# Performance work log

Hardware: AMD Instinct MI355X
Metric: run time of the kernel (lower is better)

The kernel has to match this reference:

```python
import jax, jax.numpy as jnp
import numpy as np

C = 64

def conv1x1(x, w, b):
    # x: [..., C, H, W], w: [C_out, C_in], b: [C_out]  (1x1 conv == channel mix)
    return jnp.einsum('oi,...ihw->...ohw', w, x) + b[:, None, None]

def setup_inputs() -> dict:
    key = jax.random.key(0)
    ks = jax.random.split(key, 8)
    B, N, H, W = 4, 4, 256, 256
    s = 1.0 / np.sqrt(C)
    return {
        'main_input': jax.random.normal(ks[0], (B, C, H, W), jnp.float32),
        'assist_inputs': jax.random.normal(ks[1], (N, B, C, H, W), jnp.float32),
        'wq': jax.random.normal(ks[2], (C, C), jnp.float32) * s,
        'bq': jax.random.normal(ks[3], (C,), jnp.float32) * 0.01,
        'wk': jax.random.normal(ks[4], (C, C), jnp.float32) * s,
        'bk': jax.random.normal(ks[5], (C,), jnp.float32) * 0.01,
        'wv': jax.random.normal(ks[6], (C, C), jnp.float32) * s,
        'bv': jax.random.normal(ks[7], (C,), jnp.float32) * 0.01,
    }

def reference(main_input, assist_inputs, wq, bq, wk, bk, wv, bv):
    H, W = main_input.shape[-2], main_input.shape[-1]
    q = conv1x1(main_input, wq, bq)          # [B,C,H,W]
    v = conv1x1(main_input, wv, bv)          # [B,C,H,W] (same every loop iter)
    k = conv1x1(assist_inputs, wk, bk)       # [N,B,C,H,W]
    # time-axis attention: q @ k^T over W -> [N,B,C,H,H]
    attn_t = jax.nn.softmax(jnp.einsum('bchw,nbcgw->nbchg', q, k) / jnp.sqrt(jnp.float32(H)), axis=-1)
    time_ctx = jnp.einsum('nbchg,bcgw->nbchw', attn_t, v)
    # channel(space)-axis attention: q^T @ k over H -> [N,B,C,W,W]
    attn_s = jax.nn.softmax(jnp.einsum('bchw,nbchv->nbcwv', q, k) / jnp.sqrt(jnp.float32(W)), axis=-1)
    sc_ctx = jnp.einsum('bchw,nbcwv->nbchv', v, attn_s)
    return main_input + jnp.sum(time_ctx + sc_ctx, axis=0)
```

## Files before the change

kernel.cpp:

```cpp
#include <hip/hip_runtime.h>

#define HW 65536
#define CDIM 64

typedef __attribute__((ext_vector_type(8))) short bf16x8;
typedef __attribute__((ext_vector_type(4))) float f32x4;
typedef __attribute__((ext_vector_type(4))) unsigned short u16x4;

__device__ __forceinline__ unsigned short f2bf(float x) {
    union { float f; unsigned u; } v; v.f = x;
    unsigned r = v.u + 0x7fffu + ((v.u >> 16) & 1u);
    return (unsigned short)(r >> 16);
}


__global__ __launch_bounds__(256, 2)
void proj_qv_kernel(const float* __restrict__ x,
                    const float* __restrict__ wq, const float* __restrict__ bq,
                    const float* __restrict__ wv, const float* __restrict__ bv,
                    unsigned short* __restrict__ qo, unsigned short* __restrict__ vo) {
    const int t = threadIdx.x;
    const int b = blockIdx.y;
    const int pix = blockIdx.x * 256 + t;
    const float* xp = x + (size_t)b * CDIM * HW + pix;

    float aq[CDIM], av[CDIM];
#pragma unroll
    for (int c = 0; c < CDIM; ++c) { aq[c] = bq[c]; av[c] = bv[c]; }

    for (int i = 0; i < CDIM; ++i) {
        float xv = xp[(size_t)i * HW];
#pragma unroll
        for (int c = 0; c < CDIM; ++c) {
            aq[c] = fmaf(wq[c * CDIM + i], xv, aq[c]);
            av[c] = fmaf(wv[c * CDIM + i], xv, av[c]);
        }
    }
    size_t ob = (size_t)b * CDIM * HW + pix;
#pragma unroll
    for (int c = 0; c < CDIM; ++c) {
        qo[ob + (size_t)c * HW] = f2bf(aq[c]);
        vo[ob + (size_t)c * HW] = f2bf(av[c]);
    }
}

__global__ __launch_bounds__(256, 2)
void proj_k_kernel(const float* __restrict__ x,
                   const float* __restrict__ wk, const float* __restrict__ bk,
                   unsigned short* __restrict__ ko) {
    const int t = threadIdx.x;
    const int nb = blockIdx.y;
    const int pix = blockIdx.x * 256 + t;
    const float* xp = x + (size_t)nb * CDIM * HW + pix;

    float ak[CDIM];
#pragma unroll
    for (int c = 0; c < CDIM; ++c) ak[c] = bk[c];

    for (int i = 0; i < CDIM; ++i) {
        float xv = xp[(size_t)i * HW];
#pragma unroll
        for (int c = 0; c < CDIM; ++c) ak[c] = fmaf(wk[c * CDIM + i], xv, ak[c]);
    }
    size_t ob = (size_t)nb * CDIM * HW + pix;
#pragma unroll
    for (int c = 0; c < CDIM; ++c) ko[ob + (size_t)c * HW] = f2bf(ak[c]);
}


__global__ __launch_bounds__(256)
void transpose_kernel(const unsigned short* __restrict__ src, unsigned short* __restrict__ dst) {
    __shared__ unsigned short T[64 * 72];
    const int t = threadIdx.x;
    const int sl = blockIdx.y;
    const int th = blockIdx.x >> 2, tw = blockIdx.x & 3;

    const unsigned short* s = src + (size_t)sl * HW + th * 64 * 256 + tw * 64;
#pragma unroll
    for (int it = 0; it < 2; ++it) {
        int cc = t + it * 256;
        int r = cc >> 3, j = cc & 7;
        *(bf16x8*)&T[r * 72 + j * 8] = *(const bf16x8*)&s[r * 256 + j * 8];
    }
    __syncthreads();
    unsigned short* d = dst + (size_t)sl * HW + tw * 64 * 256 + th * 64;
#pragma unroll
    for (int it = 0; it < 2; ++it) {
        int cc = t + it * 256;
        int w = cc >> 3, j = cc & 7;
        bf16x8 val;
#pragma unroll
        for (int e = 0; e < 8; ++e) val[e] = (short)T[(j * 8 + e) * 72 + w];
        *(bf16x8*)&d[w * 256 + j * 8] = val;
    }
}

#define PSTRIDE 264
#define KBOFF   67584
#define KBSTRIDE 40

__global__ __launch_bounds__(512, 2)
void attn_kernel(const unsigned short* __restrict__ q,  const unsigned short* __restrict__ qT,
                 const unsigned short* __restrict__ v,  const unsigned short* __restrict__ vT,
                 const unsigned short* __restrict__ k,  const unsigned short* __restrict__ kT,
                 const float* __restrict__ mainx, float* __restrict__ out) {
    __shared__ unsigned short lds[77824];

    const int t = threadIdx.x;
    const int wave = t >> 6, lane = t & 63;
    const int quad = lane >> 4, l16 = lane & 15;
    const int bc = blockIdx.x;

    const unsigned short* Q  = q  + (size_t)bc * HW;
    const unsigned short* QT = qT + (size_t)bc * HW;
    const unsigned short* V  = v  + (size_t)bc * HW;
    const unsigned short* VT = vT + (size_t)bc * HW;

    f32x4 oacc[2][16];
#pragma unroll
    for (int rt = 0; rt < 2; ++rt)
#pragma unroll
        for (int ct = 0; ct < 16; ++ct) oacc[rt][ct] = (f32x4){0.f, 0.f, 0.f, 0.f};

    auto stage = [&](const unsigned short* src, int col0) {
#pragma unroll
        for (int it = 0; it < 2; ++it) {
            int cc = t + it * 512;
            int r = cc >> 2, j = cc & 3;
            *(bf16x8*)&lds[KBOFF + r * KBSTRIDE + j * 8] =
                *(const bf16x8*)&src[r * 256 + col0 + j * 8];
        }
    };

    for (int n = 0; n < 4; ++n) {
        const unsigned short* K  = k  + ((size_t)n * 256 + bc) * HW;
        const unsigned short* KT = kT + ((size_t)n * 256 + bc) * HW;

        for (int rt = 0; rt < 2; ++rt) {
            f32x4 s[16];
#pragma unroll
            for (int ct = 0; ct < 16; ++ct) s[ct] = (f32x4){0.f, 0.f, 0.f, 0.f};
            const unsigned short* arow = Q + (wave * 32 + rt * 16 + l16) * 256 + quad * 8;
            for (int ks = 0; ks < 8; ++ks) {
                __syncthreads();
                stage(K, ks * 32);
                __syncthreads();
                bf16x8 a = *(const bf16x8*)&arow[ks * 32];
#pragma unroll
                for (int ct = 0; ct < 16; ++ct) {
                    bf16x8 bb = *(const bf16x8*)&lds[KBOFF + (ct * 16 + l16) * KBSTRIDE + quad * 8];
                    s[ct] = __builtin_amdgcn_mfma_f32_16x16x32_bf16(a, bb, s[ct], 0, 0, 0);
                }
            }
#pragma unroll
            for (int r = 0; r < 4; ++r) {
                float m = s[0][r];
#pragma unroll
                for (int ct = 1; ct < 16; ++ct) m = fmaxf(m, s[ct][r]);
#pragma unroll
                for (int off = 1; off < 16; off <<= 1) m = fmaxf(m, __shfl_xor(m, off, 64));
                float sum = 0.f;
#pragma unroll
                for (int ct = 0; ct < 16; ++ct) {
                    float e = __expf((s[ct][r] - m) * 0.0625f);
                    s[ct][r] = e; sum += e;
                }
#pragma unroll
                for (int off = 1; off < 16; off <<= 1) sum += __shfl_xor(sum, off, 64);
                float inv = 1.f / sum;
#pragma unroll
                for (int ct = 0; ct < 16; ++ct) s[ct][r] *= inv;
            }
            int hh = wave * 32 + rt * 16 + quad * 4;
#pragma unroll
            for (int ct = 0; ct < 16; ++ct)
#pragma unroll
                for (int r = 0; r < 4; ++r)
                    lds[(hh + r) * PSTRIDE + ct * 16 + l16] = f2bf(s[ct][r]);
        }
        __syncthreads();
        for (int gb = 0; gb < 8; ++gb) {
            __syncthreads();
            stage(VT, gb * 32);
            __syncthreads();
#pragma unroll
            for (int rt = 0; rt < 2; ++rt) {
                bf16x8 a = *(const bf16x8*)&lds[(wave * 32 + rt * 16 + l16) * PSTRIDE + gb * 32 + quad * 8];
#pragma unroll
                for (int ct = 0; ct < 16; ++ct) {
                    bf16x8 bb = *(const bf16x8*)&lds[KBOFF + (ct * 16 + l16) * KBSTRIDE + quad * 8];
                    oacc[rt][ct] = __builtin_amdgcn_mfma_f32_16x16x32_bf16(a, bb, oacc[rt][ct], 0, 0, 0);
                }
            }
        }

        for (int rt = 0; rt < 2; ++rt) {
            f32x4 s[16];
#pragma unroll
            for (int ct = 0; ct < 16; ++ct) s[ct] = (f32x4){0.f, 0.f, 0.f, 0.f};
            const unsigned short* arow = QT + (wave * 32 + rt * 16 + l16) * 256 + quad * 8;
            for (int ks = 0; ks < 8; ++ks) {
                __syncthreads();
                stage(KT, ks * 32);
                __syncthreads();
                bf16x8 a = *(const bf16x8*)&arow[ks * 32];
#pragma unroll
                for (int ct = 0; ct < 16; ++ct) {
                    bf16x8 bb = *(const bf16x8*)&lds[KBOFF + (ct * 16 + l16) * KBSTRIDE + quad * 8];
                    s[ct] = __builtin_amdgcn_mfma_f32_16x16x32_bf16(a, bb, s[ct], 0, 0, 0);
                }
            }
#pragma unroll
            for (int r = 0; r < 4; ++r) {
                float m = s[0][r];
#pragma unroll
                for (int ct = 1; ct < 16; ++ct) m = fmaxf(m, s[ct][r]);
#pragma unroll
                for (int off = 1; off < 16; off <<= 1) m = fmaxf(m, __shfl_xor(m, off, 64));
                float sum = 0.f;
#pragma unroll
                for (int ct = 0; ct < 16; ++ct) {
                    float e = __expf((s[ct][r] - m) * 0.0625f);
                    s[ct][r] = e; sum += e;
                }
#pragma unroll
                for (int off = 1; off < 16; off <<= 1) sum += __shfl_xor(sum, off, 64);
                float inv = 1.f / sum;
#pragma unroll
                for (int ct = 0; ct < 16; ++ct) s[ct][r] *= inv;
            }
            int wbase = wave * 32 + rt * 16 + quad * 4;
#pragma unroll
            for (int ct = 0; ct < 16; ++ct) {
                u16x4 pk;
#pragma unroll
                for (int r = 0; r < 4; ++r) pk[r] = f2bf(s[ct][r]);
                *(u16x4*)&lds[(ct * 16 + l16) * PSTRIDE + wbase] = pk;
            }
        }
        __syncthreads();
        for (int ks = 0; ks < 8; ++ks) {
#pragma unroll
            for (int rt = 0; rt < 2; ++rt) {
                bf16x8 a = *(const bf16x8*)&V[(wave * 32 + rt * 16 + l16) * 256 + ks * 32 + quad * 8];
#pragma unroll
                for (int ct = 0; ct < 16; ++ct) {
                    bf16x8 bb = *(const bf16x8*)&lds[(ct * 16 + l16) * PSTRIDE + ks * 32 + quad * 8];
                    oacc[rt][ct] = __builtin_amdgcn_mfma_f32_16x16x32_bf16(a, bb, oacc[rt][ct], 0, 0, 0);
                }
            }
        }
        __syncthreads();
    }

    const float* mp = mainx + (size_t)bc * HW;
    float* op = out + (size_t)bc * HW;
#pragma unroll
    for (int rt = 0; rt < 2; ++rt)
#pragma unroll
        for (int ct = 0; ct < 16; ++ct)
#pragma unroll
            for (int r = 0; r < 4; ++r) {
                int hh = wave * 32 + rt * 16 + quad * 4 + r;
                int ww = ct * 16 + l16;
                op[hh * 256 + ww] = mp[hh * 256 + ww] + oacc[rt][ct][r];
            }
}


extern "C" void kernel_launch(void* const* d_in, const int* in_sizes, int n_in,
                              void* d_out, int out_size, void* d_ws, size_t ws_size,
                              hipStream_t stream) {
    const float* mainx  = (const float*)d_in[0];
    const float* assist = (const float*)d_in[1];
    const float* wq = (const float*)d_in[2];
    const float* bq = (const float*)d_in[3];
    const float* wk = (const float*)d_in[4];
    const float* bk = (const float*)d_in[5];
    const float* wv = (const float*)d_in[6];
    const float* bv = (const float*)d_in[7];
    float* outp = (float*)d_out;

    unsigned short* ws = (unsigned short*)d_ws;
    const size_t SLICE = (size_t)16777216;
    unsigned short* Qw  = ws;
    unsigned short* QTw = ws + SLICE;
    unsigned short* Vw  = ws + 2 * SLICE;
    unsigned short* VTw = ws + 3 * SLICE;
    unsigned short* Kw  = ws + 4 * SLICE;
    unsigned short* KTw = ws + 8 * SLICE;

    proj_qv_kernel<<<dim3(256, 4), 256, 0, stream>>>(mainx, wq, bq, wv, bv, Qw, Vw);
    proj_k_kernel<<<dim3(256, 16), 256, 0, stream>>>(assist, wk, bk, Kw);

    transpose_kernel<<<dim3(16, 256), 256, 0, stream>>>(Qw, QTw);
    transpose_kernel<<<dim3(16, 256), 256, 0, stream>>>(Vw, VTw);
    transpose_kernel<<<dim3(16, 1024), 256, 0, stream>>>(Kw, KTw);

    attn_kernel<<<dim3(256), 512, 0, stream>>>(Qw, QTw, Vw, VTw, Kw, KTw, mainx, outp);
}
```

Before: 1.143 ms.

## Rewrite projections and attention with register-tiled MFMA and max-free softmax

The projection kernels are replaced by a single register-tiled kernel that keeps transposed weights in LDS and computes an 8x8 channel-by-pixel block per thread with vectorized loads. The attention kernel now splits work across waves in a 2x4 grid with 4x4 MFMA sub-tiles loaded straight from global memory, dropping the per-step LDS staging of K and its double barriers. Softmax no longer subtracts the row max: it exponentiates, accumulates partial sums through LDS, then rescales P in place. This removes barriers and the max reduction, but risks overflow if scores grow large and adds an extra LDS rescale pass.

New measurement: 1.378 ms. +20.5%, slower.

```diff
diff --git a/kernel.cpp b/kernel.cpp
--- a/kernel.cpp
+++ b/kernel.cpp
@@ -2,71 +2,78 @@
 
 #define HW 65536
 #define CDIM 64
+#define PST 264
 
 typedef __attribute__((ext_vector_type(8))) short bf16x8;
 typedef __attribute__((ext_vector_type(4))) float f32x4;
 typedef __attribute__((ext_vector_type(4))) unsigned short u16x4;
+typedef __attribute__((ext_vector_type(8))) unsigned short u16x8;
 
 __device__ __forceinline__ unsigned short f2bf(float x) {
     union { float f; unsigned u; } v; v.f = x;
     unsigned r = v.u + 0x7fffu + ((v.u >> 16) & 1u);
     return (unsigned short)(r >> 16);
 }
-
-
-__global__ __launch_bounds__(256, 2)
-void proj_qv_kernel(const float* __restrict__ x,
-                    const float* __restrict__ wq, const float* __restrict__ bq,
-                    const float* __restrict__ wv, const float* __restrict__ bv,
-                    unsigned short* __restrict__ qo, unsigned short* __restrict__ vo) {
+__device__ __forceinline__ float bf2f(unsigned short u) {
+    union { unsigned u; float f; } v; v.u = ((unsigned)u) << 16; return v.f;
+}
+
+__global__ __launch_bounds__(256, 4)
+void proj_kernel(const float* __restrict__ x, const float* __restrict__ w,
+                 const float* __restrict__ bias, unsigned short* __restrict__ o) {
+    __shared__ float WT[64 * 68];
     const int t = threadIdx.x;
-    const int b = blockIdx.y;
-    const int pix = blockIdx.x * 256 + t;
-    const float* xp = x + (size_t)b * CDIM * HW + pix;
-
-    float aq[CDIM], av[CDIM];
-#pragma unroll
-    for (int c = 0; c < CDIM; ++c) { aq[c] = bq[c]; av[c] = bv[c]; }
-
-    for (int i = 0; i < CDIM; ++i) {
-        float xv = xp[(size_t)i * HW];
-#pragma unroll
-        for (int c = 0; c < CDIM; ++c) {
-            aq[c] = fmaf(wq[c * CDIM + i], xv, aq[c]);
-            av[c] = fmaf(wv[c * CDIM + i], xv, av[c]);
-        }
-    }
-    size_t ob = (size_t)b * CDIM * HW + pix;
-#pragma unroll
-    for (int c = 0; c < CDIM; ++c) {
-        qo[ob + (size_t)c * HW] = f2bf(aq[c]);
-        vo[ob + (size_t)c * HW] = f2bf(av[c]);
-    }
-}
-
-__global__ __launch_bounds__(256, 2)
-void proj_k_kernel(const float* __restrict__ x,
-                   const float* __restrict__ wk, const float* __restrict__ bk,
-                   unsigned short* __restrict__ ko) {
-    const int t = threadIdx.x;
-    const int nb = blockIdx.y;
-    const int pix = blockIdx.x * 256 + t;
-    const float* xp = x + (size_t)nb * CDIM * HW + pix;
-
-    float ak[CDIM];
-#pragma unroll
-    for (int c = 0; c < CDIM; ++c) ak[c] = bk[c];
-
-    for (int i = 0; i < CDIM; ++i) {
-        float xv = xp[(size_t)i * HW];
-#pragma unroll
-        for (int c = 0; c < CDIM; ++c) ak[c] = fmaf(wk[c * CDIM + i], xv, ak[c]);
-    }
-    size_t ob = (size_t)nb * CDIM * HW + pix;
-#pragma unroll
-    for (int c = 0; c < CDIM; ++c) ko[ob + (size_t)c * HW] = f2bf(ak[c]);
-}
-
+    const int slice = blockIdx.y;
+    const int pixbase = blockIdx.x * 256;
+    const int tc = t >> 5, tp = t & 31;
+    const int c0 = tc * 8, p0 = pixbase + tp * 8;
+
+#pragma unroll
+    for (int it = 0; it < 16; ++it) {
+        int idx = it * 256 + t;
+        int c = idx >> 6, i = idx & 63;
+        WT[i * 68 + c] = w[idx];
+    }
+    __syncthreads();
+
+    const float* xb = x + (size_t)slice * CDIM * HW;
+    float acc[8][8];
+#pragma unroll
+    for (int cc = 0; cc < 8; ++cc) {
+        float b = bias[c0 + cc];
+#pragma unroll
+        for (int pp = 0; pp < 8; ++pp) acc[cc][pp] = b;
+    }
+
+#pragma unroll 2
+    for (int i = 0; i < 64; ++i) {
+        f32x4 x0 = *(const f32x4*)&xb[(size_t)i * HW + p0];
+        f32x4 x1 = *(const f32x4*)&xb[(size_t)i * HW + p0 + 4];
+        f32x4 w0 = *(const f32x4*)&WT[i * 68 + c0];
+        f32x4 w1 = *(const f32x4*)&WT[i * 68 + c0 + 4];
+#pragma unroll
+        for (int cc = 0; cc < 4; ++cc) {
+#pragma unroll
+            for (int pp = 0; pp < 4; ++pp) {
+                acc[cc][pp]     = fmaf(w0[cc], x0[pp], acc[cc][pp]);
+                acc[cc][pp + 4] = fmaf(w0[cc], x1[pp], acc[cc][pp + 4]);
+                acc[cc + 4][pp]     = fmaf(w1[cc], x0[pp], acc[cc + 4][pp]);
+                acc[cc + 4][pp + 4] = fmaf(w1[cc], x1[pp], acc[cc + 4][pp + 4]);
+            }
+        }
+    }
+
+    unsigned short* ob = o + (size_t)slice * CDIM * HW;
+#pragma unroll
+    for (int cc = 0; cc < 8; ++cc) {
+        u16x4 lo, hi;
+#pragma unroll
+        for (int e = 0; e < 4; ++e) { lo[e] = f2bf(acc[cc][e]); hi[e] = f2bf(acc[cc][e + 4]); }
+        size_t ob2 = (size_t)(c0 + cc) * HW + p0;
+        *(u16x4*)&ob[ob2] = lo;
+        *(u16x4*)&ob[ob2 + 4] = hi;
+    }
+}
 
 __global__ __launch_bounds__(256)
 void transpose_kernel(const unsigned short* __restrict__ src, unsigned short* __restrict__ dst) {
@@ -95,20 +102,20 @@
     }
 }
 
-#define PSTRIDE 264
-#define KBOFF   67584
-#define KBSTRIDE 40
-
 __global__ __launch_bounds__(512, 2)
 void attn_kernel(const unsigned short* __restrict__ q,  const unsigned short* __restrict__ qT,
                  const unsigned short* __restrict__ v,  const unsigned short* __restrict__ vT,
-                 const unsigned short* __restrict__ k,  const unsigned short* __restrict__ kT,
+                 const unsigned short* __restrict__ kk, const unsigned short* __restrict__ kT,
                  const float* __restrict__ mainx, float* __restrict__ out) {
-    __shared__ unsigned short lds[77824];
+    __shared__ unsigned short P[256 * PST];
+    __shared__ float stats[256 * 4];
+    __shared__ float invbuf[264];
 
     const int t = threadIdx.x;
     const int wave = t >> 6, lane = t & 63;
     const int quad = lane >> 4, l16 = lane & 15;
+    const int wr = wave >> 2, wc = wave & 3;
+    const int h0 = wc * 64;
     const int bc = blockIdx.x;
 
     const unsigned short* Q  = q  + (size_t)bc * HW;
@@ -116,141 +123,203 @@
     const unsigned short* V  = v  + (size_t)bc * HW;
     const unsigned short* VT = vT + (size_t)bc * HW;
 
-    f32x4 oacc[2][16];
+    f32x4 oacc[2][4][4];
 #pragma unroll
     for (int rt = 0; rt < 2; ++rt)
 #pragma unroll
-        for (int ct = 0; ct < 16; ++ct) oacc[rt][ct] = (f32x4){0.f, 0.f, 0.f, 0.f};
-
-    auto stage = [&](const unsigned short* src, int col0) {
-#pragma unroll
-        for (int it = 0; it < 2; ++it) {
-            int cc = t + it * 512;
-            int r = cc >> 2, j = cc & 3;
-            *(bf16x8*)&lds[KBOFF + r * KBSTRIDE + j * 8] =
-                *(const bf16x8*)&src[r * 256 + col0 + j * 8];
-        }
-    };
+        for (int mt = 0; mt < 4; ++mt)
+#pragma unroll
+            for (int nt = 0; nt < 4; ++nt) oacc[rt][mt][nt] = (f32x4){0.f, 0.f, 0.f, 0.f};
 
     for (int n = 0; n < 4; ++n) {
-        const unsigned short* K  = k  + ((size_t)n * 256 + bc) * HW;
-        const unsigned short* KT = kT + ((size_t)n * 256 + bc) * HW;
-
+        const unsigned short* K  = kk + ((size_t)(n * 256 + bc)) * HW;
+        const unsigned short* KT = kT + ((size_t)(n * 256 + bc)) * HW;
+
+        __syncthreads();
         for (int rt = 0; rt < 2; ++rt) {
-            f32x4 s[16];
-#pragma unroll
-            for (int ct = 0; ct < 16; ++ct) s[ct] = (f32x4){0.f, 0.f, 0.f, 0.f};
-            const unsigned short* arow = Q + (wave * 32 + rt * 16 + l16) * 256 + quad * 8;
+            const int band = (wr * 2 + rt) * 64;
+            f32x4 s[4][4];
+#pragma unroll
+            for (int mt = 0; mt < 4; ++mt)
+#pragma unroll
+                for (int nt = 0; nt < 4; ++nt) s[mt][nt] = (f32x4){0.f, 0.f, 0.f, 0.f};
             for (int ks = 0; ks < 8; ++ks) {
-                __syncthreads();
-                stage(K, ks * 32);
-                __syncthreads();
-                bf16x8 a = *(const bf16x8*)&arow[ks * 32];
-#pragma unroll
-                for (int ct = 0; ct < 16; ++ct) {
-                    bf16x8 bb = *(const bf16x8*)&lds[KBOFF + (ct * 16 + l16) * KBSTRIDE + quad * 8];
-                    s[ct] = __builtin_amdgcn_mfma_f32_16x16x32_bf16(a, bb, s[ct], 0, 0, 0);
+                bf16x8 a[4], bb[4];
+#pragma unroll
+                for (int mt = 0; mt < 4; ++mt)
+                    a[mt] = *(const bf16x8*)&K[(band + mt * 16 + l16) * 256 + ks * 32 + quad * 8];
+#pragma unroll
+                for (int nt = 0; nt < 4; ++nt)
+                    bb[nt] = *(const bf16x8*)&Q[(h0 + nt * 16 + l16) * 256 + ks * 32 + quad * 8];
+#pragma unroll
+                for (int mt = 0; mt < 4; ++mt)
+#pragma unroll
+                    for (int nt = 0; nt < 4; ++nt)
+                        s[mt][nt] = __builtin_amdgcn_mfma_f32_16x16x32_bf16(a[mt], bb[nt], s[mt][nt], 0, 0, 0);
+            }
+            float csum[4] = {0.f, 0.f, 0.f, 0.f};
+#pragma unroll
+            for (int mt = 0; mt < 4; ++mt)
+#pragma unroll
+                for (int nt = 0; nt < 4; ++nt) {
+                    u16x4 pk;
+#pragma unroll
+                    for (int r = 0; r < 4; ++r) {
+                        float e = __expf(s[mt][nt][r] * 0.0625f);
+                        pk[r] = f2bf(e); csum[nt] += e;
+                    }
+                    *(u16x4*)&P[(h0 + nt * 16 + l16) * PST + band + mt * 16 + quad * 4] = pk;
                 }
-            }
-#pragma unroll
-            for (int r = 0; r < 4; ++r) {
-                float m = s[0][r];
-#pragma unroll
-                for (int ct = 1; ct < 16; ++ct) m = fmaxf(m, s[ct][r]);
-#pragma unroll
-                for (int off = 1; off < 16; off <<= 1) m = fmaxf(m, __shfl_xor(m, off, 64));
-                float sum = 0.f;
-#pragma unroll
-                for (int ct = 0; ct < 16; ++ct) {
-                    float e = __expf((s[ct][r] - m) * 0.0625f);
-                    s[ct][r] = e; sum += e;
+#pragma unroll
+            for (int nt = 0; nt < 4; ++nt) {
+                csum[nt] += __shfl_xor(csum[nt], 16);
+                csum[nt] += __shfl_xor(csum[nt], 32);
+            }
+            if (quad == 0) {
+#pragma unroll
+                for (int nt = 0; nt < 4; ++nt)
+                    stats[(h0 + nt * 16 + l16) * 4 + wr * 2 + rt] = csum[nt];
+            }
+        }
+        __syncthreads();
+        if (t < 256) {
+            f32x4 s4 = *(f32x4*)&stats[t * 4];
+            invbuf[t] = 1.f / (s4[0] + s4[1] + s4[2] + s4[3]);
+        }
+        __syncthreads();
+        for (int cc = 0; cc < 17; ++cc) {
+            int idx = cc * 512 + t;
+            if (idx < 8448) {
+                int row = idx / 33;
+                int off = idx - row * 33;
+                unsigned short* pp = &P[row * PST + off * 8];
+                u16x8 a8 = *(u16x8*)pp;
+                float f = invbuf[row];
+#pragma unroll
+                for (int e = 0; e < 8; ++e) a8[e] = f2bf(bf2f(a8[e]) * f);
+                *(u16x8*)pp = a8;
+            }
+        }
+        __syncthreads();
+        for (int ks = 0; ks < 8; ++ks) {
+            bf16x8 bb[4];
+#pragma unroll
+            for (int nt = 0; nt < 4; ++nt)
+                bb[nt] = *(const bf16x8*)&P[(h0 + nt * 16 + l16) * PST + ks * 32 + quad * 8];
+#pragma unroll
+            for (int rt = 0; rt < 2; ++rt) {
+                const int band = (wr * 2 + rt) * 64;
+                bf16x8 a[4];
+#pragma unroll
+                for (int mt = 0; mt < 4; ++mt)
+                    a[mt] = *(const bf16x8*)&VT[(band + mt * 16 + l16) * 256 + ks * 32 + quad * 8];
+#pragma unroll
+                for (int mt = 0; mt < 4; ++mt)
+#pragma unroll
+                    for (int nt = 0; nt < 4; ++nt)
+                        oacc[rt][mt][nt] = __builtin_amdgcn_mfma_f32_16x16x32_bf16(a[mt], bb[nt], oacc[rt][mt][nt], 0, 0, 0);
+            }
+        }
+
+        __syncthreads();
+        for (int rt = 0; rt < 2; ++rt) {
+            const int band = (wr * 2 + rt) * 64;
+            f32x4 s[4][4];
+#pragma unroll
+            for (int mt = 0; mt < 4; ++mt)
+#pragma unroll
+                for (int nt = 0; nt < 4; ++nt) s[mt][nt] = (f32x4){0.f, 0.f, 0.f, 0.f};
+            for (int ks = 0; ks < 8; ++ks) {
+                bf16x8 a[4], bb[4];
+#pragma unroll
+                for (int mt = 0; mt < 4; ++mt)
+                    a[mt] = *(const bf16x8*)&QT[(band + mt * 16 + l16) * 256 + ks * 32 + quad * 8];
+#pragma unroll
+                for (int nt = 0; nt < 4; ++nt)
+                    bb[nt] = *(const bf16x8*)&KT[(h0 + nt * 16 + l16) * 256 + ks * 32 + quad * 8];
+#pragma unroll
+                for (int mt = 0; mt < 4; ++mt)
+#pragma unroll
+                    for (int nt = 0; nt < 4; ++nt)
+                        s[mt][nt] = __builtin_amdgcn_mfma_f32_16x16x32_bf16(a[mt], bb[nt], s[mt][nt], 0, 0, 0);
+            }
+            float rsum[4][4];
+#pragma unroll
+            for (int mt = 0; mt < 4; ++mt)
+#pragma unroll
+                for (int r = 0; r < 4; ++r) rsum[mt][r] = 0.f;
+#pragma unroll
+            for (int mt = 0; mt < 4; ++mt)
+#pragma unroll
+                for (int nt = 0; nt < 4; ++nt) {
+                    u16x4 pk;
+#pragma unroll
+                    for (int r = 0; r < 4; ++r) {
+                        float e = __expf(s[mt][nt][r] * 0.0625f);
+                        pk[r] = f2bf(e); rsum[mt][r] += e;
+                    }
+                    *(u16x4*)&P[(h0 + nt * 16 + l16) * PST + band + mt * 16 + quad * 4] = pk;
                 }
 #pragma unroll
-                for (int off = 1; off < 16; off <<= 1) sum += __shfl_xor(sum, off, 64);
-                float inv = 1.f / sum;
-#pragma unroll
-                for (int ct = 0; ct < 16; ++ct) s[ct][r] *= inv;
-            }
-            int hh = wave * 32 + rt * 16 + quad * 4;
-#pragma unroll
-            for (int ct = 0; ct < 16; ++ct)
-#pragma unroll
-                for (int r = 0; r < 4; ++r)
-                    lds[(hh + r) * PSTRIDE + ct * 16 + l16] = f2bf(s[ct][r]);
-        }
-        __syncthreads();
-        for (int gb = 0; gb < 8; ++gb) {
-            __syncthreads();
-            stage(VT, gb * 32);
-            __syncthreads();
+            for (int mt = 0; mt < 4; ++mt)
+#pragma unroll
+                for (int r = 0; r < 4; ++r) {
+                    rsum[mt][r] += __shfl_xor(rsum[mt][r], 1);
+                    rsum[mt][r] += __shfl_xor(rsum[mt][r], 2);
+                    rsum[mt][r] += __shfl_xor(rsum[mt][r], 4);
+                    rsum[mt][r] += __shfl_xor(rsum[mt][r], 8);
+                }
+            if (l16 == 0) {
+#pragma unroll
+                for (int mt = 0; mt < 4; ++mt)
+#pragma unroll
+                    for (int r = 0; r < 4; ++r)
+                        stats[(band + mt * 16 + quad * 4 + r) * 4 + wc] = rsum[mt][r];
+            }
+        }
+        __syncthreads();
+        if (t < 256) {
+            f32x4 s4 = *(f32x4*)&stats[t * 4];
+            invbuf[t] = 1.f / (s4[0] + s4[1] + s4[2] + s4[3]);
+        }
+        __syncthreads();
+        for (int cc = 0; cc < 17; ++cc) {
+            int idx = cc * 512 + t;
+            if (idx < 8448) {
+                int row = idx / 33;
+                int off = idx - row * 33;
+                unsigned short* pp = &P[row * PST + off * 8];
+                u16x8 a8 = *(u16x8*)pp;
+                f32x4 f0 = *(f32x4*)&invbuf[off * 8];
+                f32x4 f1 = *(f32x4*)&invbuf[off * 8 + 4];
+#pragma unroll
+                for (int e = 0; e < 4; ++e) {
+                    a8[e]     = f2bf(bf2f(a8[e]) * f0[e]);
+                    a8[e + 4] = f2bf(bf2f(a8[e + 4]) * f1[e]);
+                }
+                *(u16x8*)pp = a8;
+            }
+        }
+        __syncthreads();
+        for (int ks = 0; ks < 8; ++ks) {
+            bf16x8 bb[4];
+#pragma unroll
+            for (int nt = 0; nt < 4; ++nt)
+                bb[nt] = *(const bf16x8*)&V[(h0 + nt * 16 + l16) * 256 + ks * 32 + quad * 8];
 #pragma unroll
             for (int rt = 0; rt < 2; ++rt) {
-                bf16x8 a = *(const bf16x8*)&lds[(wave * 32 + rt * 16 + l16) * PSTRIDE + gb * 32 + quad * 8];
-#pragma unroll
-                for (int ct = 0; ct < 16; ++ct) {
-                    bf16x8 bb = *(const bf16x8*)&lds[KBOFF + (ct * 16 + l16) * KBSTRIDE + quad * 8];
-                    oacc[rt][ct] = __builtin_amdgcn_mfma_f32_16x16x32_bf16(a, bb, oacc[rt][ct], 0, 0, 0);
-                }
-            }
-        }
-
-        for (int rt = 0; rt < 2; ++rt) {
-            f32x4 s[16];
-#pragma unroll
-            for (int ct = 0; ct < 16; ++ct) s[ct] = (f32x4){0.f, 0.f, 0.f, 0.f};
-            const unsigned short* arow = QT + (wave * 32 + rt * 16 + l16) * 256 + quad * 8;
-            for (int ks = 0; ks < 8; ++ks) {
-                __syncthreads();
-                stage(KT, ks * 32);
-                __syncthreads();
-                bf16x8 a = *(const bf16x8*)&arow[ks * 32];
-#pragma unroll
-                for (int ct = 0; ct < 16; ++ct) {
-                    bf16x8 bb = *(const bf16x8*)&lds[KBOFF + (ct * 16 + l16) * KBSTRIDE + quad * 8];
-                    s[ct] = __builtin_amdgcn_mfma_f32_16x16x32_bf16(a, bb, s[ct], 0, 0, 0);
-                }
-            }
-#pragma unroll
-            for (int r = 0; r < 4; ++r) {
-                float m = s[0][r];
-#pragma unroll
-                for (int ct = 1; ct < 16; ++ct) m = fmaxf(m, s[ct][r]);
-#pragma unroll
-                for (int off = 1; off < 16; off <<= 1) m = fmaxf(m, __shfl_xor(m, off, 64));
-                float sum = 0.f;
-#pragma unroll
-                for (int ct = 0; ct < 16; ++ct) {
-                    float e = __expf((s[ct][r] - m) * 0.0625f);
-                    s[ct][r] = e; sum += e;
-                }
-#pragma unroll
-                for (int off = 1; off < 16; off <<= 1) sum += __shfl_xor(sum, off, 64);
-                float inv = 1.f / sum;
-#pragma unroll
-                for (int ct = 0; ct < 16; ++ct) s[ct][r] *= inv;
-            }
-            int wbase = wave * 32 + rt * 16 + quad * 4;
-#pragma unroll
-            for (int ct = 0; ct < 16; ++ct) {
-                u16x4 pk;
-#pragma unroll
-                for (int r = 0; r < 4; ++r) pk[r] = f2bf(s[ct][r]);
-                *(u16x4*)&lds[(ct * 16 + l16) * PSTRIDE + wbase] = pk;
-            }
-        }
-        __syncthreads();
-        for (int ks = 0; ks < 8; ++ks) {
-#pragma unroll
-            for (int rt = 0; rt < 2; ++rt) {
-                bf16x8 a = *(const bf16x8*)&V[(wave * 32 + rt * 16 + l16) * 256 + ks * 32 + quad * 8];
-#pragma unroll
-                for (int ct = 0; ct < 16; ++ct) {
-                    bf16x8 bb = *(const bf16x8*)&lds[(ct * 16 + l16) * PSTRIDE + ks * 32 + quad * 8];
-                    oacc[rt][ct] = __builtin_amdgcn_mfma_f32_16x16x32_bf16(a, bb, oacc[rt][ct], 0, 0, 0);
-                }
-            }
-        }
-        __syncthreads();
+                const int band = (wr * 2 + rt) * 64;
+                bf16x8 a[4];
+#pragma unroll
+                for (int mt = 0; mt < 4; ++mt)
+                    a[mt] = *(const bf16x8*)&P[(band + mt * 16 + l16) * PST + ks * 32 + quad * 8];
+#pragma unroll
+                for (int mt = 0; mt < 4; ++mt)
+#pragma unroll
+                    for (int nt = 0; nt < 4; ++nt)
+                        oacc[rt][mt][nt] = __builtin_amdgcn_mfma_f32_16x16x32_bf16(a[mt], bb[nt], oacc[rt][mt][nt], 0, 0, 0);
+            }
+        }
     }
 
     const float* mp = mainx + (size_t)bc * HW;
@@ -258,12 +327,16 @@
 #pragma unroll
     for (int rt = 0; rt < 2; ++rt)
 #pragma unroll
-        for (int ct = 0; ct < 16; ++ct)
-#pragma unroll
-            for (int r = 0; r < 4; ++r) {
-                int hh = wave * 32 + rt * 16 + quad * 4 + r;
-                int ww = ct * 16 + l16;
-                op[hh * 256 + ww] = mp[hh * 256 + ww] + oacc[rt][ct][r];
+        for (int mt = 0; mt < 4; ++mt)
+#pragma unroll
+            for (int nt = 0; nt < 4; ++nt) {
+                int xr = (wr * 2 + rt) * 64 + mt * 16 + quad * 4;
+                int hh = h0 + nt * 16 + l16;
+                f32x4 m4 = *(const f32x4*)&mp[hh * 256 + xr];
+                f32x4 o4;
+#pragma unroll
+                for (int e = 0; e < 4; ++e) o4[e] = m4[e] + oacc[rt][mt][nt][e];
+                *(f32x4*)&op[hh * 256 + xr] = o4;
             }
 }
 
@@ -290,8 +363,9 @@
     unsigned short* Kw  = ws + 4 * SLICE;
     unsigned short* KTw = ws + 8 * SLICE;
 
-    proj_qv_kernel<<<dim3(256, 4), 256, 0, stream>>>(mainx, wq, bq, wv, bv, Qw, Vw);
-    proj_k_kernel<<<dim3(256, 16), 256, 0, stream>>>(assist, wk, bk, Kw);
+    proj_kernel<<<dim3(256, 4), 256, 0, stream>>>(mainx, wq, bq, Qw);
+    proj_kernel<<<dim3(256, 4), 256, 0, stream>>>(mainx, wv, bv, Vw);
+    proj_kernel<<<dim3(256, 16), 256, 0, stream>>>(assist, wk, bk, Kw);
 
     transpose_kernel<<<dim3(16, 256), 256, 0, stream>>>(Qw, QTw);
     transpose_kernel<<<dim3(16, 256), 256, 0, stream>>>(Vw, VTw);
```
